# Optimization experiments

Hardware: AMD Instinct MI355X
Metric: run time of the kernel (lower is better)

Reference implementation:

```python
import jax, jax.numpy as jnp
import numpy as np

UNITS = 1024
INPUT_DIM = 2048
OUTPUT_DIM = 1000
EPS = 0.01
DT = 0.1
BATCH = 8192


def _kaiming_like(key, shape, fan_in):
    # matches torch kaiming_uniform_(a=sqrt(5)) bound = sqrt(6/((1+5)*fan_in)) = 1/sqrt(fan_in)
    bound = 1.0 / np.sqrt(fan_in)
    return jax.random.uniform(key, shape, jnp.float32, -bound, bound)


def setup_inputs() -> dict:
    key = jax.random.key(0)
    ks = jax.random.split(key, 12)
    x = jax.random.normal(ks[0], (BATCH, INPUT_DIM), jnp.float32)
    W_in = _kaiming_like(ks[1], (UNITS, INPUT_DIM), INPUT_DIM)
    b_in = _kaiming_like(ks[2], (UNITS,), INPUT_DIM)
    W1 = _kaiming_like(ks[3], (UNITS, UNITS), UNITS)
    b1 = _kaiming_like(ks[4], (UNITS,), UNITS)
    W2 = _kaiming_like(ks[5], (UNITS, UNITS), UNITS)
    b2 = _kaiming_like(ks[6], (UNITS,), UNITS)
    W3 = _kaiming_like(ks[7], (UNITS, UNITS), UNITS)
    b3 = _kaiming_like(ks[8], (UNITS,), UNITS)
    W_out = _kaiming_like(ks[9], (OUTPUT_DIM, UNITS), UNITS)
    b_out = _kaiming_like(ks[10], (OUTPUT_DIM,), UNITS)
    return {"x": x, "W_in": W_in, "b_in": b_in, "W1": W1, "b1": b1,
            "W2": W2, "b2": b2, "W3": W3, "b3": b3,
            "W_out": W_out, "b_out": b_out}


def transnet_layer(z, W, b):
    # z: (B, 2U). Implicit layer: A y = rhs, output = C y - rhs (== -y mathematically)
    U = W.shape[0]
    u_in, v_in = z[:, :U], z[:, U:]
    relu_u = jax.nn.relu(u_in)
    rhs_u = u_in + DT * b                      # (B, U)
    rhs_v = v_in + (DT / EPS) * relu_u         # (B, U)
    rhs = jnp.concatenate([rhs_u, rhs_v], axis=1)  # (B, 2U)
    eye = jnp.eye(U, dtype=z.dtype)
    A = jnp.block([[eye, DT * W],
                   [-DT * W.T, (1.0 + DT / EPS) * eye]])  # (2U, 2U), batch-independent
    # factor once, solve against all batch rhs columns at once
    y = jnp.linalg.solve(A, rhs.T).T           # (B, 2U)
    u, v = y[:, :U], y[:, U:]
    u_out = DT * (v @ W.T) - u_in - DT * b
    v_out = -DT * (u @ W) + (DT / EPS) * v - v_in - (DT / EPS) * relu_u
    return jnp.concatenate([u_out, v_out], axis=1)


def reference(x, W_in, b_in, W1, b1, W2, b2, W3, b3, W_out, b_out):
    z = x @ W_in.T + b_in                      # (B, U)
    z = jnp.concatenate([z, jax.nn.relu(z)], axis=1)  # (B, 2U)
    z = transnet_layer(z, W1, b1)
    z = transnet_layer(z, W2, b2)
    z = transnet_layer(z, W3, b3)
    z = z[:, :UNITS]
    logits = jax.nn.softmax(z @ W_out.T + b_out, axis=1)
    return logits
```

## Files before the change

kernel.cpp:

```cpp
#include <hip/hip_runtime.h>
#include <hip/hip_bf16.h>
#include <cstdint>


typedef __bf16 bf16;
typedef __bf16 bf16x4 __attribute__((ext_vector_type(4)));
typedef __bf16 bf16x8 __attribute__((ext_vector_type(8)));
typedef float  f32x4  __attribute__((ext_vector_type(4)));

#define C_DT    0.1f
#define C_DTEPS 10.0f
#define C_DINV  (1.0f/11.0f)
#define C_MSC   (0.01f/121.0f)

__device__ __forceinline__ void async_load16(const bf16* g, bf16* l) {
    __builtin_amdgcn_global_load_lds(
        (__attribute__((address_space(1))) void*)(g),
        (__attribute__((address_space(3))) void*)(l),
        16, 0, 0);
}

__device__ __forceinline__ void remap_block(int& bx, int& by) {
    if (gridDim.y == 64) {
        const int lin  = by * 8 + bx;
        const int xcd  = lin & 7;
        const int slot = lin >> 3;
        by = xcd * 8 + (slot & 7);
        bx = slot >> 3;
    }
}

template<int EPI>
__global__ __launch_bounds__(256, 2)
void gemm_bt(const bf16* __restrict__ A, const bf16* __restrict__ B,
             float* __restrict__ out_f,
             bf16* __restrict__ out_b1, bf16* __restrict__ out_b2,
             const float* __restrict__ e0, const float* __restrict__ e1,
             const float* __restrict__ e2, const bf16* __restrict__ eb,
             int M, int N, int K, int lda, int ldb,
             int ldf, int ld1, int ld2, float sgn,
             long zsA, long zsB, long zs1, long zs2)
{
    __shared__ __attribute__((aligned(16))) char smem[32768];
    bf16* sAe = (bf16*)smem;
    bf16* sBe = (bf16*)(smem + 16384);

    const int t    = threadIdx.x;
    const int wave = t >> 6;
    const int lane = t & 63;
    int bx = blockIdx.x, by = blockIdx.y;
    remap_block(bx, by);
    const long zb = blockIdx.z;
    A += zb * zsA;
    B += zb * zsB;
    if (out_b1) out_b1 += zb * zs1;
    if (out_b2) out_b2 += zb * zs2;

    const long row0 = (long)by * 128;
    const long col0 = (long)bx * 128;
    const int wr = wave >> 1, wc = wave & 1;

    f32x4 acc[4][4];
#pragma unroll
    for (int i = 0; i < 4; i++)
#pragma unroll
        for (int j = 0; j < 4; j++)
            acc[i][j] = f32x4{0.f, 0.f, 0.f, 0.f};

    const int  q  = t >> 2;
    const int  gp = ((t & 3) + 4 - ((q + (q >> 2)) & 3)) & 3;
    const bf16* gA = A + (row0 + q) * (long)lda + gp * 8;
    const bf16* gB = B + (col0 + q) * (long)ldb + gp * 8;

    const int l15  = lane & 15;
    const int fch  = ((lane >> 4) + l15 + (l15 >> 2)) & 3;
    const int aoff = (wr * 64 + l15) * 32 + fch * 8;
    const int boff = (wc * 64 + l15) * 32 + fch * 8;

    auto stage = [&](int buf, int k0) {
        bf16* dA = sAe + buf * 4096 + wave * 512;
        bf16* dB = sBe + buf * 4096 + wave * 512;
        async_load16(gA + k0,                     dA);
        async_load16(gA + 64 * (long)lda + k0,    dA + 2048);
        async_load16(gB + k0,                     dB);
        async_load16(gB + 64 * (long)ldb + k0,    dB + 2048);
    };

    const int nIter = K >> 5;
    stage(0, 0);
    __syncthreads();
    for (int k = 0; k < nIter; k++) {
        const int cur = k & 1;
        if (k + 1 < nIter) stage(cur ^ 1, (k + 1) << 5);

        bf16x8 af[4], bfv[4];
#pragma unroll
        for (int i = 0; i < 4; i++)
            af[i] = *(const bf16x8*)(sAe + cur * 4096 + aoff + i * 16 * 32);
#pragma unroll
        for (int j = 0; j < 4; j++)
            bfv[j] = *(const bf16x8*)(sBe + cur * 4096 + boff + j * 16 * 32);
#pragma unroll
        for (int i = 0; i < 4; i++)
#pragma unroll
            for (int j = 0; j < 4; j++)
                acc[i][j] = __builtin_amdgcn_mfma_f32_16x16x32_bf16(
                    af[i], bfv[j], acc[i][j], 0, 0, 0);

        __syncthreads();
    }

    float* epi = (float*)smem + wave * 1024;
    const int wbase = (lane >> 4) * 256 + (l15 >> 2) * 4 + (l15 & 3);

#pragma unroll
    for (int i = 0; i < 4; i++) {
#pragma unroll
        for (int j = 0; j < 4; j++)
#pragma unroll
            for (int r = 0; r < 4; r++)
                epi[wbase + r * 64 + 16 * j] = acc[i][j][r];

#pragma unroll
        for (int qq = 0; qq < 4; qq++) {
            const f32x4 a4 = ((const f32x4*)epi)[qq * 64 + lane];
            const long m = row0 + wr * 64 + i * 16 + qq * 4 + (lane >> 4);
            const long n = col0 + wc * 64 + 4 * l15;

            if (EPI == 0) {
                const f32x4 b1 = *(const f32x4*)(e1 + n);
                const f32x4 b2 = *(const f32x4*)(e2 + n);
                f32x4 tv; bf16x4 rv, hv;
#pragma unroll
                for (int e = 0; e < 4; e++) {
                    tv[e] = a4[e] + b1[e];
                    rv[e] = (bf16)(11.f * fmaxf(tv[e], 0.f));
                    hv[e] = (bf16)(tv[e] + C_DT * b2[e]);
                }
                *(f32x4*)(out_f + m * (long)ldf + n)    = tv;
                *(bf16x4*)(out_b1 + m * (long)ld1 + n)  = rv;
                *(bf16x4*)(out_b2 + m * (long)ld2 + n)  = hv;
            } else if (EPI == 1) {
                bf16x4 ov;
#pragma unroll
                for (int e = 0; e < 4; e++)
                    ov[e] = (bf16)(((m == n + e) ? C_DINV : 0.f) - C_MSC * a4[e]);
                *(bf16x4*)(out_b1 + m * (long)ld1 + n) = ov;
                *(bf16x4*)(out_b2 + m * (long)ld2 + n) = ov;
            } else if (EPI == 2) {
                bf16x4 ov;
#pragma unroll
                for (int e = 0; e < 4; e++) ov[e] = (bf16)(sgn * a4[e]);
                *(bf16x4*)(out_b1 + m * (long)ld1 + n) = ov;
            } else if (EPI == 3) {
                bf16x4 ov;
#pragma unroll
                for (int e = 0; e < 4; e++) ov[e] = (bf16)a4[e];
                *(bf16x4*)(out_b1 + m * (long)ld1 + n) = ov;
            } else if (EPI == 4) {
                const f32x4  u0 = *(const f32x4*)(e0 + m * (long)ldf + n);
                const f32x4  b1 = *(const f32x4*)(e1 + n);
                const f32x4  b2 = *(const f32x4*)(e2 + n);
                const bf16x4 vv = *(const bf16x4*)(eb + m * (long)N + n);
                f32x4 un; bf16x4 rv, hv;
#pragma unroll
                for (int e = 0; e < 4; e++) {
                    un[e] = C_DT * a4[e] - u0[e] - C_DT * b1[e];
                    rv[e] = (bf16)(C_DTEPS * fmaxf(un[e], 0.f) - (float)vv[e]);
                    hv[e] = (bf16)(un[e] + C_DT * b2[e]);
                }
                *(f32x4*)(out_f + m * (long)ldf + n)    = un;
                *(bf16x4*)(out_b1 + m * (long)ld1 + n)  = rv;
                *(bf16x4*)(out_b2 + m * (long)ld2 + n)  = hv;
            } else {
                const f32x4 u0 = *(const f32x4*)(e0 + m * (long)ldf + n);
                const f32x4 b1 = *(const f32x4*)(e1 + n);
                bf16x4 hv, lv;
#pragma unroll
                for (int e = 0; e < 4; e++) {
                    float un = C_DT * a4[e] - u0[e] - C_DT * b1[e];
                    bf16 h = (bf16)un;
                    hv[e] = h;
                    lv[e] = (bf16)(un - (float)h);
                }
                *(bf16x4*)(out_b1 + m * (long)ld1 + n) = hv;
                *(bf16x4*)(out_b2 + m * (long)ld2 + n) = lv;
            }
        }
    }
}

__global__ __launch_bounds__(256, 2)
void gemm_split(const bf16* __restrict__ Ah, const bf16* __restrict__ Al,
                const bf16* __restrict__ Bh, const bf16* __restrict__ Bl,
                float* __restrict__ out, const float* __restrict__ bias,
                int M, int N, int K, int blim)
{
    __shared__ __attribute__((aligned(16))) char smem[65536];
    bf16* sAh = (bf16*)smem;
    bf16* sAl = (bf16*)(smem + 16384);
    bf16* sBh = (bf16*)(smem + 32768);
    bf16* sBl = (bf16*)(smem + 49152);

    const int t    = threadIdx.x;
    const int wave = t >> 6;
    const int lane = t & 63;
    int bx = blockIdx.x, by = blockIdx.y;
    remap_block(bx, by);
    const long row0 = (long)by * 128;
    const long col0 = (long)bx * 128;
    const int wr = wave >> 1, wc = wave & 1;

    f32x4 acc[4][4];
#pragma unroll
    for (int i = 0; i < 4; i++)
#pragma unroll
        for (int j = 0; j < 4; j++)
            acc[i][j] = f32x4{0.f, 0.f, 0.f, 0.f};

    const int  q  = t >> 2;
    const int  gp = ((t & 3) + 4 - ((q + (q >> 2)) & 3)) & 3;
    const long gao = (row0 + q) * (long)K + gp * 8;
    const long gbo = (col0 + q) * (long)K + gp * 8;

    const int l15  = lane & 15;
    const int fch  = ((lane >> 4) + l15 + (l15 >> 2)) & 3;
    const int aoff = (wr * 64 + l15) * 32 + fch * 8;
    const int boff = (wc * 64 + l15) * 32 + fch * 8;

    auto stage = [&](int buf, int k0) {
        const int d = buf * 4096 + wave * 512;
        async_load16(Ah + gao + k0,                 sAh + d);
        async_load16(Ah + gao + 64 * (long)K + k0,  sAh + d + 2048);
        async_load16(Al + gao + k0,                 sAl + d);
        async_load16(Al + gao + 64 * (long)K + k0,  sAl + d + 2048);
        async_load16(Bh + gbo + k0,                 sBh + d);
        async_load16(Bh + gbo + 64 * (long)K + k0,  sBh + d + 2048);
        async_load16(Bl + gbo + k0,                 sBl + d);
        async_load16(Bl + gbo + 64 * (long)K + k0,  sBl + d + 2048);
    };

    const int nIter = K >> 5;
    stage(0, 0);
    __syncthreads();
    for (int k = 0; k < nIter; k++) {
        const int cur = k & 1;
        if (k + 1 < nIter) stage(cur ^ 1, (k + 1) << 5);

        bf16x8 ah[4], al[4], bh[4], bl[4];
#pragma unroll
        for (int i = 0; i < 4; i++) {
            ah[i] = *(const bf16x8*)(sAh + cur * 4096 + aoff + i * 16 * 32);
            al[i] = *(const bf16x8*)(sAl + cur * 4096 + aoff + i * 16 * 32);
        }
#pragma unroll
        for (int j = 0; j < 4; j++) {
            bh[j] = *(const bf16x8*)(sBh + cur * 4096 + boff + j * 16 * 32);
            bl[j] = *(const bf16x8*)(sBl + cur * 4096 + boff + j * 16 * 32);
        }
#pragma unroll
        for (int i = 0; i < 4; i++)
#pragma unroll
            for (int j = 0; j < 4; j++) {
                acc[i][j] = __builtin_amdgcn_mfma_f32_16x16x32_bf16(
                    ah[i], bh[j], acc[i][j], 0, 0, 0);
                acc[i][j] = __builtin_amdgcn_mfma_f32_16x16x32_bf16(
                    ah[i], bl[j], acc[i][j], 0, 0, 0);
                acc[i][j] = __builtin_amdgcn_mfma_f32_16x16x32_bf16(
                    al[i], bh[j], acc[i][j], 0, 0, 0);
            }
        __syncthreads();
    }

    float* epi = (float*)smem + wave * 1024;
    const int wbase = (lane >> 4) * 256 + (l15 >> 2) * 4 + (l15 & 3);

#pragma unroll
    for (int i = 0; i < 4; i++) {
#pragma unroll
        for (int j = 0; j < 4; j++)
#pragma unroll
            for (int r = 0; r < 4; r++)
                epi[wbase + r * 64 + 16 * j] = acc[i][j][r];

#pragma unroll
        for (int qq = 0; qq < 4; qq++) {
            f32x4 a4 = ((const f32x4*)epi)[qq * 64 + lane];
            const long m = row0 + wr * 64 + i * 16 + qq * 4 + (lane >> 4);
            const long n = col0 + wc * 64 + 4 * l15;
            f32x4 bv = f32x4{0.f, 0.f, 0.f, 0.f};
            if (n < blim) bv = *(const f32x4*)(bias + n);
#pragma unroll
            for (int e = 0; e < 4; e++) a4[e] += bv[e];
            *(f32x4*)(out + m * (long)N + n) = a4;
        }
    }
}

__global__ void conv_xw(const float* __restrict__ x, bf16* __restrict__ xb,
                        const float* __restrict__ w, bf16* __restrict__ wb)
{
    const long bid = blockIdx.x;
    const float* in;
    bf16* outp;
    long i4;
    if (bid < 16384) { in = x; outp = xb; i4 = bid * 256 + threadIdx.x; }
    else             { in = w; outp = wb; i4 = (bid - 16384) * 256 + threadIdx.x; }
    const f32x4 v = ((const f32x4*)in)[i4];
    bf16x4 o;
#pragma unroll
    for (int e = 0; e < 4; e++) o[e] = (bf16)v[e];
    ((bf16x4*)outp)[i4] = o;
}

__global__ void prep_w3(const float* __restrict__ w0, const float* __restrict__ w1,
                        const float* __restrict__ w2, bf16* __restrict__ Wb,
                        bf16* __restrict__ Wtb)
{
    __shared__ float tile[32][33];
    const int z = blockIdx.z;
    const float* W = (z == 0) ? w0 : (z == 1) ? w1 : w2;
    const long zo = (long)z * 1024 * 1024;
    const int bx = blockIdx.x * 32, by = blockIdx.y * 32;
    const int tx = threadIdx.x & 31, ty = threadIdx.x >> 5;
#pragma unroll
    for (int i = 0; i < 32; i += 8) {
        float v = W[(long)(by + ty + i) * 1024 + bx + tx];
        tile[ty + i][tx] = v;
        Wb[zo + (long)(by + ty + i) * 1024 + bx + tx] = (bf16)v;
    }
    __syncthreads();
#pragma unroll
    for (int i = 0; i < 32; i += 8)
        Wtb[zo + (long)(bx + ty + i) * 1024 + by + tx] = (bf16)tile[tx][ty + i];
}

__global__ void prep_wout(const float* __restrict__ w, bf16* __restrict__ wh,
                          bf16* __restrict__ wl)
{
    const long i4   = (long)blockIdx.x * 256 + threadIdx.x;
    const long base = i4 * 4;
    const int  nrow = (int)(base >> 10);
    bf16x4 h, l;
    if (nrow < 1000) {
        const f32x4 v = ((const f32x4*)w)[i4];
#pragma unroll
        for (int e = 0; e < 4; e++) {
            bf16 hh = (bf16)v[e];
            h[e] = hh;
            l[e] = (bf16)(v[e] - (float)hh);
        }
    } else {
#pragma unroll
        for (int e = 0; e < 4; e++) { h[e] = (bf16)0.f; l[e] = (bf16)0.f; }
    }
    ((bf16x4*)wh)[i4] = h;
    ((bf16x4*)wl)[i4] = l;
}

__global__ __launch_bounds__(256)
void softmax_rows(const float* __restrict__ logits, float* __restrict__ out)
{
    const int row = blockIdx.x;
    const float* lp = logits + (long)row * 1024;
    const int t = threadIdx.x;
    float v[4];
    float mx = -1e30f;
#pragma unroll
    for (int i = 0; i < 4; i++) {
        const int c = t + i * 256;
        v[i] = (c < 1000) ? lp[c] : -1e30f;
        mx = fmaxf(mx, v[i]);
    }
#pragma unroll
    for (int off = 32; off; off >>= 1)
        mx = fmaxf(mx, __shfl_xor(mx, off));
    __shared__ float sm[4], ss[4];
    const int wave = t >> 6;
    if ((t & 63) == 0) sm[wave] = mx;
    __syncthreads();
    mx = fmaxf(fmaxf(sm[0], sm[1]), fmaxf(sm[2], sm[3]));
    float sum = 0.f;
#pragma unroll
    for (int i = 0; i < 4; i++) {
        v[i] = __expf(v[i] - mx);
        sum += v[i];
    }
#pragma unroll
    for (int off = 32; off; off >>= 1)
        sum += __shfl_xor(sum, off);
    if ((t & 63) == 0) ss[wave] = sum;
    __syncthreads();
    const float inv = 1.f / (ss[0] + ss[1] + ss[2] + ss[3]);
#pragma unroll
    for (int i = 0; i < 4; i++) {
        const int c = t + i * 256;
        if (c < 1000) out[(long)row * 1000 + c] = v[i] * inv;
    }
}

extern "C" void kernel_launch(void* const* d_in, const int* in_sizes, int n_in,
                              void* d_out, int out_size, void* d_ws, size_t ws_size,
                              hipStream_t stream)
{
    const float* x     = (const float*)d_in[0];
    const float* W_in  = (const float*)d_in[1];
    const float* b_in  = (const float*)d_in[2];
    const float* Ws[3] = {(const float*)d_in[3], (const float*)d_in[5], (const float*)d_in[7]};
    const float* bs[3] = {(const float*)d_in[4], (const float*)d_in[6], (const float*)d_in[8]};
    const float* W_out = (const float*)d_in[9];
    const float* b_out = (const float*)d_in[10];
    float* out = (float*)d_out;

    char* ws = (char*)d_ws;
    const size_t MB = 1u << 20;
    const long M1 = 1024L * 1024;
    bf16*  xb       = (bf16*)(ws);
    bf16*  Wtbf_all = (bf16*)(ws);
    bf16*  Minv_all = (bf16*)(ws +  6 * MB);
    bf16*  Bcat_all = (bf16*)(ws + 12 * MB);
    bf16*  Wbf_all  = (bf16*)(ws + 24 * MB);
    bf16*  Winb  = (bf16*)(ws + 32 * MB);
    bf16*  Wouth = (bf16*)(ws + 36 * MB);
    bf16*  Woutl = (bf16*)(ws + 38 * MB);
    float* u_a   = (float*)(ws + 40 * MB);
    float* u_b   = (float*)(ws + 72 * MB);
    bf16*  AC    = (bf16*)(ws + 104 * MB);
    bf16*  vb    = (bf16*)(ws + 136 * MB);
    bf16*  zh    = AC;
    bf16*  zl    = AC + 8192L * 1024;
    float* logits = u_b;

    const dim3 blk(256);
    const dim3 gBig(8, 64);
    const dim3 gSm3(8, 8, 3);
    const dim3 gT3(32, 32, 3);

    conv_xw<<<18432, blk, 0, stream>>>(x, xb, W_in, Winb);
    prep_wout<<<1024, blk, 0, stream>>>(W_out, Wouth, Woutl);

    gemm_bt<0><<<gBig, blk, 0, stream>>>(xb, Winb, u_a, AC, AC + 1024,
                                         nullptr, b_in, bs[0], nullptr,
                                         8192, 1024, 2048, 2048, 2048,
                                         1024, 2048, 2048, 1.f, 0, 0, 0, 0);

    prep_w3<<<gT3, blk, 0, stream>>>(Ws[0], Ws[1], Ws[2], Wbf_all, Wtbf_all);
    gemm_bt<1><<<gSm3, blk, 0, stream>>>(Wtbf_all, Wtbf_all, nullptr, Minv_all, Bcat_all,
                                         nullptr, nullptr, nullptr, nullptr,
                                         1024, 1024, 1024, 1024, 1024,
                                         0, 1024, 2048, 1.f, M1, M1, M1, 2 * M1);
    gemm_bt<2><<<gSm3, blk, 0, stream>>>(Minv_all, Wbf_all, nullptr, Bcat_all + 1024, nullptr,
                                         nullptr, nullptr, nullptr, nullptr,
                                         1024, 1024, 1024, 1024, 1024,
                                         0, 2048, 0, C_DT, M1, M1, 2 * M1, 0);

    float* uin[3]  = {u_a, u_b, u_a};
    float* uout[3] = {u_b, u_a, nullptr};
    for (int l = 0; l < 3; l++) {
        gemm_bt<3><<<gBig, blk, 0, stream>>>(AC, Bcat_all + l * 2 * M1, nullptr, vb, nullptr,
                                             nullptr, nullptr, nullptr, nullptr,
                                             8192, 1024, 2048, 2048, 2048,
                                             0, 1024, 0, 1.f, 0, 0, 0, 0);
        if (l < 2) {
            gemm_bt<4><<<gBig, blk, 0, stream>>>(vb, Wbf_all + l * M1, uout[l], AC, AC + 1024,
                                                 uin[l], bs[l], bs[l + 1], vb,
                                                 8192, 1024, 1024, 1024, 1024,
                                                 1024, 2048, 2048, 1.f, 0, 0, 0, 0);
        } else {
            gemm_bt<5><<<gBig, blk, 0, stream>>>(vb, Wbf_all + l * M1, nullptr, zh, zl,
                                                 uin[l], bs[l], nullptr, nullptr,
                                                 8192, 1024, 1024, 1024, 1024,
                                                 1024, 1024, 1024, 1.f, 0, 0, 0, 0);
        }
    }

    gemm_split<<<gBig, blk, 0, stream>>>(zh, zl, Wouth, Woutl, logits, b_out,
                                         8192, 1024, 1024, 1000);
    softmax_rows<<<8192, blk, 0, stream>>>(logits, out);
}
```

Before: 529.1 us.

## Fold per-layer second GEMM into precomputed weight product and fuse dual-output layer GEMM

Before the batch loop, the weight products W·Minv and its composition with W are precomputed, giving a second concatenated matrix Ccat per layer. Each layer's two chained batch GEMMs (v, then u from v) become a single K=2048 pass that computes both V and U accumulators from one shared A tile. This removes a full 8192x1024x1024 GEMM per layer plus the intermediate vb round trip. In exchange it adds small weight-only GEMMs, doubles the accumulator registers per block, and may change rounding because the product is stored in bf16.

```diff
diff --git a/kernel.cpp b/kernel.cpp
--- a/kernel.cpp
+++ b/kernel.cpp
@@ -36,7 +36,7 @@
              float* __restrict__ out_f,
              bf16* __restrict__ out_b1, bf16* __restrict__ out_b2,
              const float* __restrict__ e0, const float* __restrict__ e1,
-             const float* __restrict__ e2, const bf16* __restrict__ eb,
+             const float* __restrict__ e2,
              int M, int N, int K, int lda, int ldb,
              int ldf, int ld1, int ld2, float sgn,
              long zsA, long zsB, long zs1, long zs2)
@@ -148,37 +148,21 @@
                 *(bf16x4*)(out_b1 + m * (long)ld1 + n) = ov;
                 *(bf16x4*)(out_b2 + m * (long)ld2 + n) = ov;
             } else if (EPI == 2) {
-                bf16x4 ov;
-#pragma unroll
-                for (int e = 0; e < 4; e++) ov[e] = (bf16)(sgn * a4[e]);
+                bf16x4 ov, o2;
+#pragma unroll
+                for (int e = 0; e < 4; e++) {
+                    ov[e] = (bf16)(sgn * a4[e]);
+                    o2[e] = (bf16)(C_DT * sgn * a4[e]);
+                }
                 *(bf16x4*)(out_b1 + m * (long)ld1 + n) = ov;
-            } else if (EPI == 3) {
-                bf16x4 ov;
-#pragma unroll
-                for (int e = 0; e < 4; e++) ov[e] = (bf16)a4[e];
-                *(bf16x4*)(out_b1 + m * (long)ld1 + n) = ov;
-            } else if (EPI == 4) {
-                const f32x4  u0 = *(const f32x4*)(e0 + m * (long)ldf + n);
-                const f32x4  b1 = *(const f32x4*)(e1 + n);
-                const f32x4  b2 = *(const f32x4*)(e2 + n);
-                const bf16x4 vv = *(const bf16x4*)(eb + m * (long)N + n);
-                f32x4 un; bf16x4 rv, hv;
-#pragma unroll
-                for (int e = 0; e < 4; e++) {
-                    un[e] = C_DT * a4[e] - u0[e] - C_DT * b1[e];
-                    rv[e] = (bf16)(C_DTEPS * fmaxf(un[e], 0.f) - (float)vv[e]);
-                    hv[e] = (bf16)(un[e] + C_DT * b2[e]);
-                }
-                *(f32x4*)(out_f + m * (long)ldf + n)    = un;
-                *(bf16x4*)(out_b1 + m * (long)ld1 + n)  = rv;
-                *(bf16x4*)(out_b2 + m * (long)ld2 + n)  = hv;
+                if (out_b2) *(bf16x4*)(out_b2 + m * (long)ld2 + n) = o2;
             } else {
                 const f32x4 u0 = *(const f32x4*)(e0 + m * (long)ldf + n);
                 const f32x4 b1 = *(const f32x4*)(e1 + n);
                 bf16x4 hv, lv;
 #pragma unroll
                 for (int e = 0; e < 4; e++) {
-                    float un = C_DT * a4[e] - u0[e] - C_DT * b1[e];
+                    float un = sgn * a4[e] - u0[e] - C_DT * b1[e];
                     bf16 h = (bf16)un;
                     hv[e] = h;
                     lv[e] = (bf16)(un - (float)h);
@@ -186,6 +170,128 @@
                 *(bf16x4*)(out_b1 + m * (long)ld1 + n) = hv;
                 *(bf16x4*)(out_b2 + m * (long)ld2 + n) = lv;
             }
+        }
+    }
+}
+
+__global__ __launch_bounds__(256, 2)
+void gemm_layer(const bf16* __restrict__ A, const bf16* __restrict__ B1,
+                const bf16* __restrict__ B2, float* __restrict__ u,
+                bf16* __restrict__ ACo,
+                const float* __restrict__ bl, const float* __restrict__ bn)
+{
+    __shared__ __attribute__((aligned(16))) char smem[49152];
+    bf16* sA  = (bf16*)smem;
+    bf16* sB1 = (bf16*)(smem + 16384);
+    bf16* sB2 = (bf16*)(smem + 32768);
+
+    const int t    = threadIdx.x;
+    const int wave = t >> 6;
+    const int lane = t & 63;
+    int bx = blockIdx.x, by = blockIdx.y;
+    remap_block(bx, by);
+    const long row0 = (long)by * 128;
+    const long col0 = (long)bx * 128;
+    const int wr = wave >> 1, wc = wave & 1;
+
+    f32x4 accU[4][4], accV[4][4];
+#pragma unroll
+    for (int i = 0; i < 4; i++)
+#pragma unroll
+        for (int j = 0; j < 4; j++) {
+            accU[i][j] = f32x4{0.f, 0.f, 0.f, 0.f};
+            accV[i][j] = f32x4{0.f, 0.f, 0.f, 0.f};
+        }
+
+    const int  q  = t >> 2;
+    const int  gp = ((t & 3) + 4 - ((q + (q >> 2)) & 3)) & 3;
+    const bf16* gA  = A  + (row0 + q) * 2048 + gp * 8;
+    const bf16* gB1 = B1 + (col0 + q) * 2048 + gp * 8;
+    const bf16* gB2 = B2 + (col0 + q) * 2048 + gp * 8;
+
+    const int l15  = lane & 15;
+    const int fch  = ((lane >> 4) + l15 + (l15 >> 2)) & 3;
+    const int aoff = (wr * 64 + l15) * 32 + fch * 8;
+    const int boff = (wc * 64 + l15) * 32 + fch * 8;
+
+    auto stage = [&](int buf, int k0) {
+        bf16* dA  = sA  + buf * 4096 + wave * 512;
+        bf16* dB1 = sB1 + buf * 4096 + wave * 512;
+        bf16* dB2 = sB2 + buf * 4096 + wave * 512;
+        async_load16(gA  + k0,             dA);
+        async_load16(gA  + 64 * 2048 + k0, dA + 2048);
+        async_load16(gB1 + k0,             dB1);
+        async_load16(gB1 + 64 * 2048 + k0, dB1 + 2048);
+        async_load16(gB2 + k0,             dB2);
+        async_load16(gB2 + 64 * 2048 + k0, dB2 + 2048);
+    };
+
+    stage(0, 0);
+    __syncthreads();
+    for (int k = 0; k < 64; k++) {
+        const int cur = k & 1;
+        if (k + 1 < 64) stage(cur ^ 1, (k + 1) << 5);
+
+        bf16x8 af[4], b1v[4], b2v[4];
+#pragma unroll
+        for (int i = 0; i < 4; i++)
+            af[i] = *(const bf16x8*)(sA + cur * 4096 + aoff + i * 16 * 32);
+#pragma unroll
+        for (int j = 0; j < 4; j++) {
+            b1v[j] = *(const bf16x8*)(sB1 + cur * 4096 + boff + j * 16 * 32);
+            b2v[j] = *(const bf16x8*)(sB2 + cur * 4096 + boff + j * 16 * 32);
+        }
+#pragma unroll
+        for (int i = 0; i < 4; i++)
+#pragma unroll
+            for (int j = 0; j < 4; j++) {
+                accV[i][j] = __builtin_amdgcn_mfma_f32_16x16x32_bf16(
+                    af[i], b1v[j], accV[i][j], 0, 0, 0);
+                accU[i][j] = __builtin_amdgcn_mfma_f32_16x16x32_bf16(
+                    af[i], b2v[j], accU[i][j], 0, 0, 0);
+            }
+        __syncthreads();
+    }
+
+    float* epi = (float*)smem + wave * 1024;
+    const int wbase = (lane >> 4) * 256 + (l15 >> 2) * 4 + (l15 & 3);
+
+#pragma unroll
+    for (int i = 0; i < 4; i++) {
+#pragma unroll
+        for (int j = 0; j < 4; j++)
+#pragma unroll
+            for (int r = 0; r < 4; r++)
+                epi[wbase + r * 64 + 16 * j] = accV[i][j][r];
+        f32x4 v4[4];
+#pragma unroll
+        for (int qq = 0; qq < 4; qq++)
+            v4[qq] = ((const f32x4*)epi)[qq * 64 + lane];
+#pragma unroll
+        for (int j = 0; j < 4; j++)
+#pragma unroll
+            for (int r = 0; r < 4; r++)
+                epi[wbase + r * 64 + 16 * j] = accU[i][j][r];
+
+#pragma unroll
+        for (int qq = 0; qq < 4; qq++) {
+            const f32x4 a4 = ((const f32x4*)epi)[qq * 64 + lane];
+            const long m  = row0 + wr * 64 + i * 16 + qq * 4 + (lane >> 4);
+            const long n  = col0 + wc * 64 + 4 * l15;
+            const long iu = m * 1024 + n;
+            const f32x4 u0 = *(const f32x4*)(u + iu);
+            const f32x4 c1 = *(const f32x4*)(bl + n);
+            const f32x4 c2 = *(const f32x4*)(bn + n);
+            f32x4 un; bf16x4 rv, hv;
+#pragma unroll
+            for (int e = 0; e < 4; e++) {
+                un[e] = a4[e] - u0[e] - C_DT * c1[e];
+                rv[e] = (bf16)(C_DTEPS * fmaxf(un[e], 0.f) - v4[qq][e]);
+                hv[e] = (bf16)(un[e] + C_DT * c2[e]);
+            }
+            *(f32x4*)(u + iu) = un;
+            *(bf16x4*)(ACo + m * 2048 + n)        = rv;
+            *(bf16x4*)(ACo + m * 2048 + 1024 + n) = hv;
         }
     }
 }
@@ -415,21 +521,22 @@
     char* ws = (char*)d_ws;
     const size_t MB = 1u << 20;
     const long M1 = 1024L * 1024;
-    bf16*  xb       = (bf16*)(ws);
-    bf16*  Wtbf_all = (bf16*)(ws);
-    bf16*  Minv_all = (bf16*)(ws +  6 * MB);
-    bf16*  Bcat_all = (bf16*)(ws + 12 * MB);
-    bf16*  Wbf_all  = (bf16*)(ws + 24 * MB);
+    bf16*  xb    = (bf16*)(ws);
+    bf16*  Wtbf  = (bf16*)(ws);
+    bf16*  Minv  = (bf16*)(ws +  6 * MB);
+    bf16*  Pmat  = (bf16*)(ws + 12 * MB);
+    bf16*  Bcat  = (bf16*)(ws + 18 * MB);
+    bf16*  zh    = (bf16*)(ws);
+    bf16*  zl    = (bf16*)(ws + 16 * MB);
     bf16*  Winb  = (bf16*)(ws + 32 * MB);
     bf16*  Wouth = (bf16*)(ws + 36 * MB);
     bf16*  Woutl = (bf16*)(ws + 38 * MB);
-    float* u_a   = (float*)(ws + 40 * MB);
-    float* u_b   = (float*)(ws + 72 * MB);
-    bf16*  AC    = (bf16*)(ws + 104 * MB);
-    bf16*  vb    = (bf16*)(ws + 136 * MB);
-    bf16*  zh    = AC;
-    bf16*  zl    = AC + 8192L * 1024;
-    float* logits = u_b;
+    bf16*  Wbf   = (bf16*)(ws + 40 * MB);
+    bf16*  Ccat  = (bf16*)(ws + 46 * MB);
+    float* u     = (float*)(ws + 58 * MB);
+    float* logits= (float*)(ws + 58 * MB);
+    bf16*  AC_a  = (bf16*)(ws + 90 * MB);
+    bf16*  AC_b  = (bf16*)(ws + 122 * MB);
 
     const dim3 blk(256);
     const dim3 gBig(8, 64);
@@ -439,40 +546,36 @@
     conv_xw<<<18432, blk, 0, stream>>>(x, xb, W_in, Winb);
     prep_wout<<<1024, blk, 0, stream>>>(W_out, Wouth, Woutl);
 
-    gemm_bt<0><<<gBig, blk, 0, stream>>>(xb, Winb, u_a, AC, AC + 1024,
-                                         nullptr, b_in, bs[0], nullptr,
+    gemm_bt<0><<<gBig, blk, 0, stream>>>(xb, Winb, u, AC_a, AC_a + 1024,
+                                         nullptr, b_in, bs[0],
                                          8192, 1024, 2048, 2048, 2048,
                                          1024, 2048, 2048, 1.f, 0, 0, 0, 0);
 
-    prep_w3<<<gT3, blk, 0, stream>>>(Ws[0], Ws[1], Ws[2], Wbf_all, Wtbf_all);
-    gemm_bt<1><<<gSm3, blk, 0, stream>>>(Wtbf_all, Wtbf_all, nullptr, Minv_all, Bcat_all,
-                                         nullptr, nullptr, nullptr, nullptr,
+    prep_w3<<<gT3, blk, 0, stream>>>(Ws[0], Ws[1], Ws[2], Wbf, Wtbf);
+    gemm_bt<1><<<gSm3, blk, 0, stream>>>(Wtbf, Wtbf, nullptr, Minv, Bcat,
+                                         nullptr, nullptr, nullptr,
                                          1024, 1024, 1024, 1024, 1024,
                                          0, 1024, 2048, 1.f, M1, M1, M1, 2 * M1);
-    gemm_bt<2><<<gSm3, blk, 0, stream>>>(Minv_all, Wbf_all, nullptr, Bcat_all + 1024, nullptr,
-                                         nullptr, nullptr, nullptr, nullptr,
+    gemm_bt<2><<<gSm3, blk, 0, stream>>>(Minv, Wbf, nullptr, Bcat + 1024, nullptr,
+                                         nullptr, nullptr, nullptr,
                                          1024, 1024, 1024, 1024, 1024,
                                          0, 2048, 0, C_DT, M1, M1, 2 * M1, 0);
-
-    float* uin[3]  = {u_a, u_b, u_a};
-    float* uout[3] = {u_b, u_a, nullptr};
-    for (int l = 0; l < 3; l++) {
-        gemm_bt<3><<<gBig, blk, 0, stream>>>(AC, Bcat_all + l * 2 * M1, nullptr, vb, nullptr,
-                                             nullptr, nullptr, nullptr, nullptr,
-                                             8192, 1024, 2048, 2048, 2048,
-                                             0, 1024, 0, 1.f, 0, 0, 0, 0);
-        if (l < 2) {
-            gemm_bt<4><<<gBig, blk, 0, stream>>>(vb, Wbf_all + l * M1, uout[l], AC, AC + 1024,
-                                                 uin[l], bs[l], bs[l + 1], vb,
-                                                 8192, 1024, 1024, 1024, 1024,
-                                                 1024, 2048, 2048, 1.f, 0, 0, 0, 0);
-        } else {
-            gemm_bt<5><<<gBig, blk, 0, stream>>>(vb, Wbf_all + l * M1, nullptr, zh, zl,
-                                                 uin[l], bs[l], nullptr, nullptr,
-                                                 8192, 1024, 1024, 1024, 1024,
-                                                 1024, 1024, 1024, 1.f, 0, 0, 0, 0);
-        }
-    }
+    gemm_bt<2><<<gSm3, blk, 0, stream>>>(Wbf, Minv, nullptr, Pmat, Ccat,
+                                         nullptr, nullptr, nullptr,
+                                         1024, 1024, 1024, 1024, 1024,
+                                         0, 1024, 2048, 1.f, M1, M1, M1, 2 * M1);
+    gemm_bt<2><<<gSm3, blk, 0, stream>>>(Pmat, Wbf, nullptr, Ccat + 1024, nullptr,
+                                         nullptr, nullptr, nullptr,
+                                         1024, 1024, 1024, 1024, 1024,
+                                         0, 2048, 0, 0.01f, M1, M1, 2 * M1, 0);
+
+    gemm_layer<<<gBig, blk, 0, stream>>>(AC_a, Bcat, Ccat, u, AC_b, bs[0], bs[1]);
+    gemm_layer<<<gBig, blk, 0, stream>>>(AC_b, Bcat + 2 * M1, Ccat + 2 * M1,
+                                         u, AC_a, bs[1], bs[2]);
+    gemm_bt<5><<<gBig, blk, 0, stream>>>(AC_a, Ccat + 4 * M1, nullptr, zh, zl,
+                                         u, bs[2], nullptr,
+                                         8192, 1024, 2048, 2048, 2048,
+                                         1024, 1024, 1024, 1.f, 0, 0, 0, 0);
 
     gemm_split<<<gBig, blk, 0, stream>>>(zh, zl, Wouth, Woutl, logits, b_out,
                                          8192, 1024, 1024, 1000);
```

New measurement: 527.0 us. Within noise of the previous version (-0.4%).
